# Kernel optimization log

Measured on AMD Instinct MI355X. Metric: run time of the kernel, lower is better.

## Reference

```python
import jax, jax.numpy as jnp
import numpy as np

B, D, H, C = 512, 1024, 512, 4


def setup_inputs() -> dict:
    key = jax.random.key(0)
    k_x, k_v, k_w = jax.random.split(key, 3)
    # x holds categorical values in [0, C) used as float multipliers
    x = jax.random.randint(k_x, (B, D), 0, C).astype(jnp.float32)
    # xavier_normal_ per torch fan computation: V fan_in=D*C, fan_out=H*C; W fan_in=D, fan_out=H
    V = jax.random.normal(k_v, (H, D, C), jnp.float32) * np.float32(np.sqrt(2.0 / (D * C + H * C)))
    b = jnp.zeros((D, C), jnp.float32)
    W = jax.random.normal(k_w, (H, D), jnp.float32) * np.float32(np.sqrt(2.0 / (D + H)))
    c = jnp.zeros((1, H), jnp.float32)
    return {"x": x, "V": V, "b": b, "W": W, "c": c}


def _nade_forward(x, V, b, W, c):
    Bsz = x.shape[0]
    a0 = jnp.broadcast_to(c, (Bsz, c.shape[1]))  # [B, H]
    # per-step slices stacked along leading D axis for lax.scan
    xs = (jnp.transpose(V, (1, 0, 2)),  # [D, H, C]
          b,                            # [D, C]
          W.T,                          # [D, H]
          x.T)                          # [D, B]

    def step(a, inp):
        V_d, b_d, w_d, x_d = inp
        h = jax.nn.sigmoid(a)                 # [B, H]
        logits = h @ V_d + b_d                # [B, C]
        p = jax.nn.log_softmax(logits, axis=1)
        a_new = a + x_d[:, None] * w_d[None, :]  # rank-1 update of running preactivation
        return a_new, (logits, p)

    _, (logits, p) = jax.lax.scan(step, a0, xs)   # each [D, B, C]
    y_hat = jnp.transpose(logits, (1, 0, 2)).reshape(Bsz, -1)  # [B, D*C], d-major blocks of size C
    p_hat = jnp.transpose(p, (1, 0, 2)).reshape(Bsz, -1)
    return y_hat, p_hat


def reference(x, V, b, W, c):
    return _nade_forward(x, V, b, W, c)
```

## Files before the change

kernel.cpp:

```cpp
#include <hip/hip_runtime.h>
#include <hip/hip_fp16.h>


#define Bv 512
#define Dv 1024
#define Hv 512
#define Cv 4
#define Kv 64
#define DCv 16

#define L2E 1.4426950408889634f
#define LN2 0.6931471805599453f

typedef __attribute__((ext_vector_type(8))) short short8;
typedef __attribute__((ext_vector_type(4))) float f32x4;
typedef __attribute__((ext_vector_type(2))) float v2f;

__device__ __forceinline__ float fexp2(float x) { return __builtin_amdgcn_exp2f(x); }
__device__ __forceinline__ float flog2(float x) { return __builtin_amdgcn_logf(x); }
__device__ __forceinline__ float frcp(float x)  { return __builtin_amdgcn_rcpf(x); }

__device__ __forceinline__ v2f fma2(v2f a, v2f b, v2f c) {
#if __has_builtin(__builtin_elementwise_fma)
    return __builtin_elementwise_fma(a, b, c);
#else
    v2f r; r.x = fmaf(a.x, b.x, c.x); r.y = fmaf(a.y, b.y, c.y); return r;
#endif
}

__device__ __forceinline__ unsigned bf16pk(float lo, float hi) {
    return __builtin_amdgcn_perm(__float_as_uint(hi), __float_as_uint(lo), 0x07060302u);
}
__device__ __forceinline__ unsigned short bf16rne(float f) {
    unsigned u = __float_as_uint(f);
    return (unsigned short)((u + 0x7FFFu + ((u >> 16) & 1u)) >> 16);
}

__global__ __launch_bounds__(256) void k_prep_all(
        const float* __restrict__ V, const float* __restrict__ W,
        const float* __restrict__ x, unsigned short* __restrict__ VtA4,
        float* __restrict__ WtL, float* __restrict__ xt) {
    __shared__ char smem[17408];
    const int bid = blockIdx.x;
    if (bid < 256) {
        unsigned short* tile = (unsigned short*)smem;
        const int d0 = bid * 4;
        const int dd = threadIdx.x & 3;
        const int hb0 = threadIdx.x >> 2;
#pragma unroll
        for (int p = 0; p < 8; ++p) {
            int h = p * 64 + hb0;
            float4 v = *(const float4*)(V + ((size_t)h * Dv + d0 + dd) * Cv);
            int hb = h >> 5, q = (h >> 3) & 3, j = h & 7;
            int base = ((dd * 16 + hb) * 16 + q * 4) * 8 + j;
            tile[base + 0]  = bf16rne(v.x);
            tile[base + 8]  = bf16rne(v.y);
            tile[base + 16] = bf16rne(v.z);
            tile[base + 24] = bf16rne(v.w);
        }
        __syncthreads();
        uint4* dst = (uint4*)(VtA4 + (size_t)d0 * 2048);
        const uint4* src = (const uint4*)tile;
        for (int t = threadIdx.x; t < 1024; t += 256) dst[t] = src[t];
    } else {
        float (*t)[65] = (float (*)[65])smem;
        const int mb   = (bid - 256) >> 7;
        const int tile = (bid - 256) & 127;
        const int tr   = tile >> 4;
        const int tc   = tile & 15;
        const float* src = mb ? x : W;
        float* dst       = mb ? xt : WtL;
        const float scale = mb ? 1.0f : L2E;
        const int lx = threadIdx.x & 15;
        const int ly = threadIdx.x >> 4;
#pragma unroll
        for (int r = 0; r < 64; r += 16) {
            int row = r + ly;
            float4 v = *(const float4*)(src + (size_t)(tr * 64 + row) * Dv + tc * 64 + lx * 4);
            t[row][lx * 4 + 0] = v.x;
            t[row][lx * 4 + 1] = v.y;
            t[row][lx * 4 + 2] = v.z;
            t[row][lx * 4 + 3] = v.w;
        }
        __syncthreads();
#pragma unroll
        for (int r = 0; r < 64; r += 16) {
            int row = r + ly;
            float4 o = make_float4(t[lx * 4 + 0][row] * scale,
                                   t[lx * 4 + 1][row] * scale,
                                   t[lx * 4 + 2][row] * scale,
                                   t[lx * 4 + 3][row] * scale);
            *(float4*)(dst + (size_t)(tc * 64 + row) * 512 + tr * 64 + lx * 4) = o;
        }
    }
}

__global__ __launch_bounds__(512) void k_partial(const float* __restrict__ x,
                          const float* __restrict__ WtL, __half* __restrict__ P) {
    int k  = blockIdx.x >> 6;
    int bg = blockIdx.x & 63;
    int h  = threadIdx.x;
    int d0 = k * DCv;

    __shared__ float xs[DCv * 8];
    if (threadIdx.x < DCv * 8) {
        int g = threadIdx.x & 7;
        int j = threadIdx.x >> 3;
        xs[j * 8 + g] = x[(size_t)(bg * 8 + g) * Dv + d0 + j];
    }
    __syncthreads();

    float acc[8];
#pragma unroll
    for (int g = 0; g < 8; ++g) acc[g] = 0.0f;

    const float* wp = WtL + (size_t)d0 * Hv + h;
#pragma unroll
    for (int j = 0; j < DCv; ++j) {
        float wv = wp[(size_t)j * Hv];
        const float4 x0 = *(const float4*)(xs + j * 8);
        const float4 x1 = *(const float4*)(xs + j * 8 + 4);
        acc[0] = fmaf(x0.x, wv, acc[0]);
        acc[1] = fmaf(x0.y, wv, acc[1]);
        acc[2] = fmaf(x0.z, wv, acc[2]);
        acc[3] = fmaf(x0.w, wv, acc[3]);
        acc[4] = fmaf(x1.x, wv, acc[4]);
        acc[5] = fmaf(x1.y, wv, acc[5]);
        acc[6] = fmaf(x1.z, wv, acc[6]);
        acc[7] = fmaf(x1.w, wv, acc[7]);
    }
#pragma unroll
    for (int g = 0; g < 8; ++g)
        P[((size_t)k * Bv + bg * 8 + g) * Hv + h] = __float2half(acc[g]);
}

__global__ void k_prefix(__half* __restrict__ A0, const float* __restrict__ cbias) {
    int gid = blockIdx.x * blockDim.x + threadIdx.x;
    int h = gid & (Hv - 1);
    int bi = gid >> 9;
    float run = cbias[h] * L2E;
    __half* p = A0 + (size_t)bi * Hv + h;
#pragma unroll 4
    for (int k = 0; k < Kv; ++k) {
        float t = __half2float(p[(size_t)k * Bv * Hv]);
        p[(size_t)k * Bv * Hv] = __float2half(run);
        run += t;
    }
}

__global__ __launch_bounds__(128) void k_main(
        const float* __restrict__ xt, const float* __restrict__ bbias,
        const unsigned short* __restrict__ VtA4, const float* __restrict__ WtL,
        const __half* __restrict__ A0, float* __restrict__ out) {
    const int k    = blockIdx.x >> 5;
    const int bg   = blockIdx.x & 31;
    const int wv   = threadIdx.x >> 6;
    const int lane = threadIdx.x & 63;
    const int bl   = lane & 15;
    const int quad = lane >> 4;
    const int b    = bg * 16 + bl;
    const int d0   = k * DCv;

    __shared__ f32x4 red[2][2][2][64];

    v2f a2[32];
    {
        const __half* ap = A0 + ((size_t)k * Bv + b) * Hv + wv * 256 + quad * 8;
#pragma unroll
        for (int kb = 0; kb < 8; ++kb) {
            union { uint4 u; __half2 h2[4]; } t;
            t.u = *(const uint4*)(ap + kb * 32);
#pragma unroll
            for (int tt = 0; tt < 4; ++tt) {
                float2 f = __half22float2(t.h2[tt]);
                a2[kb * 4 + tt] = (v2f){f.x, f.y};
            }
        }
    }

    const int blc = (bl < 4) ? bl : 0;
    const unsigned short* vp = VtA4 + (((size_t)d0 * 16 + wv * 8) * 16 + quad * 4 + blc) * 8;
    const float* wp = WtL + (size_t)d0 * Hv + wv * 256 + quad * 8;
    const float* xp = xt + (size_t)d0 * Bv + b;
    const float* bp = bbias + (d0 + wv) * Cv;
    float* sy = out + (size_t)b * Dv * Cv + (d0 + wv) * Cv;
    float* spp = sy + (size_t)Bv * Dv * Cv;

    for (int i1 = 0; i1 < DCv / 2; ++i1) {
        float xdA = xp[0];
        float xdB = xp[Bv];
        float4 bbv = *(const float4*)bp;

        f32x4 accA = {0.f, 0.f, 0.f, 0.f};
#pragma unroll
        for (int kb = 0; kb < 8; ++kb) {
            union { unsigned u[4]; short8 s; } cv;
#pragma unroll
            for (int t = 0; t < 4; ++t) {
                v2f aa = a2[kb * 4 + t];
                v2f e; e.x = fexp2(-aa.x); e.y = fexp2(-aa.y);
                v2f q = e + 1.0f;
                cv.u[t] = bf16pk(frcp(q.x), frcp(q.y));
            }
            short8 af = *(const short8*)(vp + kb * 128);
            accA = __builtin_amdgcn_mfma_f32_16x16x32_bf16(af, cv.s, accA, 0, 0, 0);
        }
        v2f xA2 = {xdA, xdA};
#pragma unroll
        for (int kb = 0; kb < 8; ++kb) {
            float4 w0 = *(const float4*)(wp + kb * 32);
            float4 w1 = *(const float4*)(wp + kb * 32 + 4);
            a2[kb*4+0] = fma2(xA2, (v2f){w0.x, w0.y}, a2[kb*4+0]);
            a2[kb*4+1] = fma2(xA2, (v2f){w0.z, w0.w}, a2[kb*4+1]);
            a2[kb*4+2] = fma2(xA2, (v2f){w1.x, w1.y}, a2[kb*4+2]);
            a2[kb*4+3] = fma2(xA2, (v2f){w1.z, w1.w}, a2[kb*4+3]);
        }

        f32x4 accB = {0.f, 0.f, 0.f, 0.f};
#pragma unroll
        for (int kb = 0; kb < 8; ++kb) {
            union { unsigned u[4]; short8 s; } cv;
#pragma unroll
            for (int t = 0; t < 4; ++t) {
                v2f aa = a2[kb * 4 + t];
                v2f e; e.x = fexp2(-aa.x); e.y = fexp2(-aa.y);
                v2f q = e + 1.0f;
                cv.u[t] = bf16pk(frcp(q.x), frcp(q.y));
            }
            short8 af = *(const short8*)(vp + 2048 + kb * 128);
            accB = __builtin_amdgcn_mfma_f32_16x16x32_bf16(af, cv.s, accB, 0, 0, 0);
        }
        v2f xB2 = {xdB, xdB};
#pragma unroll
        for (int kb = 0; kb < 8; ++kb) {
            float4 w0 = *(const float4*)(wp + Hv + kb * 32);
            float4 w1 = *(const float4*)(wp + Hv + kb * 32 + 4);
            a2[kb*4+0] = fma2(xB2, (v2f){w0.x, w0.y}, a2[kb*4+0]);
            a2[kb*4+1] = fma2(xB2, (v2f){w0.z, w0.w}, a2[kb*4+1]);
            a2[kb*4+2] = fma2(xB2, (v2f){w1.x, w1.y}, a2[kb*4+2]);
            a2[kb*4+3] = fma2(xB2, (v2f){w1.z, w1.w}, a2[kb*4+3]);
        }

        red[i1 & 1][0][wv][lane] = accA;
        red[i1 & 1][1][wv][lane] = accB;
        __syncthreads();

        f32x4 s = red[i1 & 1][wv][0][lane] + red[i1 & 1][wv][1][lane];
        float w0 = s.x + bbv.x;
        float w1 = s.y + bbv.y;
        float w2 = s.z + bbv.z;
        float w3 = s.w + bbv.w;
        float mx = fmaxf(fmaxf(w0, w1), fmaxf(w2, w3));
        float e0 = fexp2((w0 - mx) * L2E);
        float e1 = fexp2((w1 - mx) * L2E);
        float e2 = fexp2((w2 - mx) * L2E);
        float e3 = fexp2((w3 - mx) * L2E);
        float lse = mx + flog2(e0 + e1 + e2 + e3) * LN2;
        if (quad == 0) {
            *(float4*)sy  = make_float4(w0, w1, w2, w3);
            *(float4*)spp = make_float4(w0 - lse, w1 - lse, w2 - lse, w3 - lse);
        }

        vp += 2 * 2048;
        wp += 2 * Hv;
        xp += 2 * Bv;
        bp += 2 * Cv;
        sy += 2 * Cv;
        spp += 2 * Cv;
    }
}

extern "C" void kernel_launch(void* const* d_in, const int* in_sizes, int n_in,
                              void* d_out, int out_size, void* d_ws, size_t ws_size,
                              hipStream_t stream) {
    const float* x  = (const float*)d_in[0];
    const float* V  = (const float*)d_in[1];
    const float* bb = (const float*)d_in[2];
    const float* W  = (const float*)d_in[3];
    const float* cb = (const float*)d_in[4];
    float* out = (float*)d_out;

    char* ws = (char*)d_ws;
    unsigned short* VtA4 = (unsigned short*)ws;
    float* WtL = (float*)(ws + (size_t)4 * 1024 * 1024);
    float* xt  = (float*)(ws + (size_t)6 * 1024 * 1024);
    __half* A0 = (__half*)(ws + (size_t)8 * 1024 * 1024);

    k_prep_all<<<512, 256, 0, stream>>>(V, W, x, VtA4, WtL, xt);
    k_partial<<<Kv * (Bv / 8), 512, 0, stream>>>(x, WtL, A0);
    k_prefix<<<(Bv * Hv) / 256, 256, 0, stream>>>(A0, cb);
    k_main<<<Kv * 32, 128, 0, stream>>>(xt, bb, VtA4, WtL, A0, out);
}
```

Measured before the change: 175.4 us.

## Fuse partial-sum kernel into prep, use bit-trick reciprocal sigmoid, split MFMA accumulators

Merges k_partial into the prep kernel so it reads W directly instead of waiting on the transposed WtL, which drops one launch and removes the dependency between the two. The prep blocks now use 512 threads. In the main loop, sigmoid now uses an integer-bit reciprocal guess plus one Newton step in place of the hardware rcp, and each chain of MFMAs alternates between two accumulators to shorten the dependency chain. The approximate reciprocal may lose accuracy, though the result is rounded to bf16 anyway.

```diff
diff --git a/kernel.cpp b/kernel.cpp
--- a/kernel.cpp
+++ b/kernel.cpp
@@ -28,6 +28,14 @@
 #endif
 }
 
+__device__ __forceinline__ float sig1t(float a) {
+    float e = fexp2(-a);
+    float q = 1.0f + e;
+    float r0 = __int_as_float(0x7EF311C3 - __float_as_int(q));
+    float t = fmaf(-q, r0, 2.0f);
+    return r0 * t;
+}
+
 __device__ __forceinline__ unsigned bf16pk(float lo, float hi) {
     return __builtin_amdgcn_perm(__float_as_uint(hi), __float_as_uint(lo), 0x07060302u);
 }
@@ -36,10 +44,11 @@
     return (unsigned short)((u + 0x7FFFu + ((u >> 16) & 1u)) >> 16);
 }
 
-__global__ __launch_bounds__(256) void k_prep_all(
+__global__ __launch_bounds__(512) void k_prep(
         const float* __restrict__ V, const float* __restrict__ W,
         const float* __restrict__ x, unsigned short* __restrict__ VtA4,
-        float* __restrict__ WtL, float* __restrict__ xt) {
+        float* __restrict__ WtL, float* __restrict__ xt,
+        __half* __restrict__ P) {
     __shared__ char smem[17408];
     const int bid = blockIdx.x;
     if (bid < 256) {
@@ -48,8 +57,8 @@
         const int dd = threadIdx.x & 3;
         const int hb0 = threadIdx.x >> 2;
 #pragma unroll
-        for (int p = 0; p < 8; ++p) {
-            int h = p * 64 + hb0;
+        for (int p = 0; p < 4; ++p) {
+            int h = p * 128 + hb0;
             float4 v = *(const float4*)(V + ((size_t)h * Dv + d0 + dd) * Cv);
             int hb = h >> 5, q = (h >> 3) & 3, j = h & 7;
             int base = ((dd * 16 + hb) * 16 + q * 4) * 8 + j;
@@ -61,8 +70,10 @@
         __syncthreads();
         uint4* dst = (uint4*)(VtA4 + (size_t)d0 * 2048);
         const uint4* src = (const uint4*)tile;
-        for (int t = threadIdx.x; t < 1024; t += 256) dst[t] = src[t];
-    } else {
+#pragma unroll
+        for (int p = 0; p < 2; ++p)
+            dst[p * 512 + threadIdx.x] = src[p * 512 + threadIdx.x];
+    } else if (bid < 512) {
         float (*t)[65] = (float (*)[65])smem;
         const int mb   = (bid - 256) >> 7;
         const int tile = (bid - 256) & 127;
@@ -74,7 +85,7 @@
         const int lx = threadIdx.x & 15;
         const int ly = threadIdx.x >> 4;
 #pragma unroll
-        for (int r = 0; r < 64; r += 16) {
+        for (int r = 0; r < 64; r += 32) {
             int row = r + ly;
             float4 v = *(const float4*)(src + (size_t)(tr * 64 + row) * Dv + tc * 64 + lx * 4);
             t[row][lx * 4 + 0] = v.x;
@@ -84,7 +95,7 @@
         }
         __syncthreads();
 #pragma unroll
-        for (int r = 0; r < 64; r += 16) {
+        for (int r = 0; r < 64; r += 32) {
             int row = r + ly;
             float4 o = make_float4(t[lx * 4 + 0][row] * scale,
                                    t[lx * 4 + 1][row] * scale,
@@ -92,46 +103,47 @@
                                    t[lx * 4 + 3][row] * scale);
             *(float4*)(dst + (size_t)(tc * 64 + row) * 512 + tr * 64 + lx * 4) = o;
         }
+    } else {
+        float* xs = (float*)smem;
+        const int pb = bid - 512;
+        const int k  = pb >> 6;
+        const int bg = pb & 63;
+        const int h  = threadIdx.x;
+        const int d0 = k * DCv;
+        if (threadIdx.x < DCv * 8) {
+            int g = threadIdx.x & 7;
+            int j = threadIdx.x >> 3;
+            xs[j * 8 + g] = x[(size_t)(bg * 8 + g) * Dv + d0 + j];
+        }
+        __syncthreads();
+
+        float wr[DCv];
+        const float* wp = W + (size_t)h * Dv + d0;
+#pragma unroll
+        for (int j4 = 0; j4 < DCv; j4 += 4)
+            *(float4*)(wr + j4) = *(const float4*)(wp + j4);
+
+        float acc[8];
+#pragma unroll
+        for (int g = 0; g < 8; ++g) acc[g] = 0.0f;
+#pragma unroll
+        for (int j = 0; j < DCv; ++j) {
+            float wv = wr[j];
+            const float4 x0 = *(const float4*)(xs + j * 8);
+            const float4 x1 = *(const float4*)(xs + j * 8 + 4);
+            acc[0] = fmaf(x0.x, wv, acc[0]);
+            acc[1] = fmaf(x0.y, wv, acc[1]);
+            acc[2] = fmaf(x0.z, wv, acc[2]);
+            acc[3] = fmaf(x0.w, wv, acc[3]);
+            acc[4] = fmaf(x1.x, wv, acc[4]);
+            acc[5] = fmaf(x1.y, wv, acc[5]);
+            acc[6] = fmaf(x1.z, wv, acc[6]);
+            acc[7] = fmaf(x1.w, wv, acc[7]);
+        }
+#pragma unroll
+        for (int g = 0; g < 8; ++g)
+            P[((size_t)k * Bv + bg * 8 + g) * Hv + h] = __float2half(acc[g] * L2E);
     }
-}
-
-__global__ __launch_bounds__(512) void k_partial(const float* __restrict__ x,
-                          const float* __restrict__ WtL, __half* __restrict__ P) {
-    int k  = blockIdx.x >> 6;
-    int bg = blockIdx.x & 63;
-    int h  = threadIdx.x;
-    int d0 = k * DCv;
-
-    __shared__ float xs[DCv * 8];
-    if (threadIdx.x < DCv * 8) {
-        int g = threadIdx.x & 7;
-        int j = threadIdx.x >> 3;
-        xs[j * 8 + g] = x[(size_t)(bg * 8 + g) * Dv + d0 + j];
-    }
-    __syncthreads();
-
-    float acc[8];
-#pragma unroll
-    for (int g = 0; g < 8; ++g) acc[g] = 0.0f;
-
-    const float* wp = WtL + (size_t)d0 * Hv + h;
-#pragma unroll
-    for (int j = 0; j < DCv; ++j) {
-        float wv = wp[(size_t)j * Hv];
-        const float4 x0 = *(const float4*)(xs + j * 8);
-        const float4 x1 = *(const float4*)(xs + j * 8 + 4);
-        acc[0] = fmaf(x0.x, wv, acc[0]);
-        acc[1] = fmaf(x0.y, wv, acc[1]);
-        acc[2] = fmaf(x0.z, wv, acc[2]);
-        acc[3] = fmaf(x0.w, wv, acc[3]);
-        acc[4] = fmaf(x1.x, wv, acc[4]);
-        acc[5] = fmaf(x1.y, wv, acc[5]);
-        acc[6] = fmaf(x1.z, wv, acc[6]);
-        acc[7] = fmaf(x1.w, wv, acc[7]);
-    }
-#pragma unroll
-    for (int g = 0; g < 8; ++g)
-        P[((size_t)k * Bv + bg * 8 + g) * Hv + h] = __float2half(acc[g]);
 }
 
 __global__ void k_prefix(__half* __restrict__ A0, const float* __restrict__ cbias) {
@@ -191,20 +203,23 @@
         float xdB = xp[Bv];
         float4 bbv = *(const float4*)bp;
 
-        f32x4 accA = {0.f, 0.f, 0.f, 0.f};
+        f32x4 acc0 = {0.f, 0.f, 0.f, 0.f};
+        f32x4 acc1 = {0.f, 0.f, 0.f, 0.f};
 #pragma unroll
         for (int kb = 0; kb < 8; ++kb) {
             union { unsigned u[4]; short8 s; } cv;
 #pragma unroll
             for (int t = 0; t < 4; ++t) {
                 v2f aa = a2[kb * 4 + t];
-                v2f e; e.x = fexp2(-aa.x); e.y = fexp2(-aa.y);
-                v2f q = e + 1.0f;
-                cv.u[t] = bf16pk(frcp(q.x), frcp(q.y));
+                cv.u[t] = bf16pk(sig1t(aa.x), sig1t(aa.y));
             }
             short8 af = *(const short8*)(vp + kb * 128);
-            accA = __builtin_amdgcn_mfma_f32_16x16x32_bf16(af, cv.s, accA, 0, 0, 0);
-        }
+            if (kb & 1)
+                acc1 = __builtin_amdgcn_mfma_f32_16x16x32_bf16(af, cv.s, acc1, 0, 0, 0);
+            else
+                acc0 = __builtin_amdgcn_mfma_f32_16x16x32_bf16(af, cv.s, acc0, 0, 0, 0);
+        }
+        f32x4 accA = acc0 + acc1;
         v2f xA2 = {xdA, xdA};
 #pragma unroll
         for (int kb = 0; kb < 8; ++kb) {
@@ -216,20 +231,23 @@
             a2[kb*4+3] = fma2(xA2, (v2f){w1.z, w1.w}, a2[kb*4+3]);
         }
 
-        f32x4 accB = {0.f, 0.f, 0.f, 0.f};
+        f32x4 acc2 = {0.f, 0.f, 0.f, 0.f};
+        f32x4 acc3 = {0.f, 0.f, 0.f, 0.f};
 #pragma unroll
         for (int kb = 0; kb < 8; ++kb) {
             union { unsigned u[4]; short8 s; } cv;
 #pragma unroll
             for (int t = 0; t < 4; ++t) {
                 v2f aa = a2[kb * 4 + t];
-                v2f e; e.x = fexp2(-aa.x); e.y = fexp2(-aa.y);
-                v2f q = e + 1.0f;
-                cv.u[t] = bf16pk(frcp(q.x), frcp(q.y));
+                cv.u[t] = bf16pk(sig1t(aa.x), sig1t(aa.y));
             }
             short8 af = *(const short8*)(vp + 2048 + kb * 128);
-            accB = __builtin_amdgcn_mfma_f32_16x16x32_bf16(af, cv.s, accB, 0, 0, 0);
-        }
+            if (kb & 1)
+                acc3 = __builtin_amdgcn_mfma_f32_16x16x32_bf16(af, cv.s, acc3, 0, 0, 0);
+            else
+                acc2 = __builtin_amdgcn_mfma_f32_16x16x32_bf16(af, cv.s, acc2, 0, 0, 0);
+        }
+        f32x4 accB = acc2 + acc3;
         v2f xB2 = {xdB, xdB};
 #pragma unroll
         for (int kb = 0; kb < 8; ++kb) {
@@ -286,8 +304,7 @@
     float* xt  = (float*)(ws + (size_t)6 * 1024 * 1024);
     __half* A0 = (__half*)(ws + (size_t)8 * 1024 * 1024);
 
-    k_prep_all<<<512, 256, 0, stream>>>(V, W, x, VtA4, WtL, xt);
-    k_partial<<<Kv * (Bv / 8), 512, 0, stream>>>(x, WtL, A0);
+    k_prep<<<512 + Kv * (Bv / 8), 512, 0, stream>>>(V, W, x, VtA4, WtL, xt, A0);
     k_prefix<<<(Bv * Hv) / 256, 256, 0, stream>>>(A0, cb);
     k_main<<<Kv * 32, 128, 0, stream>>>(xt, bb, VtA4, WtL, A0, out);
 }
```

After: 186.7 us. 1.06x slower.
